# Kernel optimization log

Hardware: AMD Instinct MI355X
Metric: run time of the kernel (lower is better)

## Reference

```python
import jax, jax.numpy as jnp
import numpy as np

N = 102400   # total nodes (256 graphs x 400 nodes)
E = 1600000  # total edges
B = 256      # number of graphs
F_IN = 4
H = 128
GH = 120     # GRU hidden
C_IN = 84
L = 100


def setup_inputs() -> dict:
    key = jax.random.key(0)
    ks = jax.random.split(key, 32)
    rn = lambda k, shape, sc: (jax.random.normal(k, shape, jnp.float32) * sc)
    s = lambda fan: 1.0 / np.sqrt(fan)
    inp = {}
    inp["x"] = rn(ks[0], (N, F_IN), 1.0)
    inp["edge_index"] = jax.random.randint(ks[1], (2, E), 0, N)
    inp["batch"] = jnp.repeat(jnp.arange(B), N // B)  # sorted segment ids, no empty segments
    inp["target01"] = rn(ks[2], (B, C_IN, L), 1.0)
    # GraphConv params: out = segsum(x_j) @ W_rel + b + x @ W_root
    inp["W1_rel"] = rn(ks[3], (F_IN, H), s(F_IN)); inp["W1_root"] = rn(ks[4], (F_IN, H), s(F_IN)); inp["b1"] = jnp.zeros((H,), jnp.float32)
    inp["W2_rel"] = rn(ks[5], (H, H), s(H)); inp["W2_root"] = rn(ks[6], (H, H), s(H)); inp["b2"] = jnp.zeros((H,), jnp.float32)
    inp["W3_rel"] = rn(ks[7], (H, H), s(H)); inp["W3_root"] = rn(ks[8], (H, H), s(H)); inp["b3"] = jnp.zeros((H,), jnp.float32)
    # Conv1d(84 -> 128, k=3)
    inp["Wc"] = rn(ks[9], (H, C_IN, 3), s(C_IN * 3)); inp["bc"] = jnp.zeros((H,), jnp.float32)
    # Bidirectional GRU(128 -> 120)
    inp["Wih_f"] = rn(ks[10], (3 * GH, H), s(H)); inp["Whh_f"] = rn(ks[11], (3 * GH, GH), s(GH))
    inp["bih_f"] = jnp.zeros((3 * GH,), jnp.float32); inp["bhh_f"] = jnp.zeros((3 * GH,), jnp.float32)
    inp["Wih_b"] = rn(ks[12], (3 * GH, H), s(H)); inp["Whh_b"] = rn(ks[13], (3 * GH, GH), s(GH))
    inp["bih_b"] = jnp.zeros((3 * GH,), jnp.float32); inp["bhh_b"] = jnp.zeros((3 * GH,), jnp.float32)
    # Dense head
    inp["Wd1"] = rn(ks[14], (4816, 102), s(4816)); inp["bd1"] = jnp.zeros((102,), jnp.float32)
    inp["Wd3"] = rn(ks[15], (102, 2), s(102)); inp["bd3"] = jnp.zeros((2,), jnp.float32)
    return inp


def _graph_conv(x, src, dst, W_rel, b, W_root, n):
    # PyG GraphConv, aggr='add': lin_rel(sum_j x_j) + lin_root(x)
    agg = jax.ops.segment_sum(x[src], dst, num_segments=n)
    return agg @ W_rel + b + x @ W_root


def _gru_dir(xs, Wih, Whh, bih, bhh, reverse):
    # xs: [T, B, D] -> [T, B, GH]; PyTorch GRU cell equations
    h0 = jnp.zeros((xs.shape[1], Whh.shape[1]), xs.dtype)
    def step(h, xt):
        gi = xt @ Wih.T + bih
        gh = h @ Whh.T + bhh
        ir, iz, i_n = jnp.split(gi, 3, axis=-1)
        hr, hz, h_n = jnp.split(gh, 3, axis=-1)
        r = jax.nn.sigmoid(ir + hr)
        z = jax.nn.sigmoid(iz + hz)
        n = jnp.tanh(i_n + r * h_n)
        h2 = (1.0 - z) * n + z * h
        return h2, h2
    _, ys = jax.lax.scan(step, h0, xs, reverse=reverse)
    return ys


def reference(x, edge_index, batch, target01, W1_rel, W1_root, b1, W2_rel, W2_root, b2,
              W3_rel, W3_root, b3, Wc, bc, Wih_f, Whh_f, bih_f, bhh_f,
              Wih_b, Whh_b, bih_b, bhh_b, Wd1, bd1, Wd3, bd3):
    src, dst = edge_index[0], edge_index[1]
    n = x.shape[0]
    x1 = jax.nn.relu(_graph_conv(x, src, dst, W1_rel, b1, W1_root, n))
    x2 = jax.nn.relu(_graph_conv(x1, src, dst, W2_rel, b2, W2_root, n))
    x3 = jax.nn.relu(_graph_conv(x2, src, dst, W3_rel, b3, W3_root, n)) + x1  # residual
    x4 = jax.nn.relu(_graph_conv(x3, src, dst, W3_rel, b3, W3_root, n))      # conv3 reused
    gmax = jax.ops.segment_max(x4, batch, num_segments=B)
    gsum = jax.ops.segment_sum(x4, batch, num_segments=B)
    cnt = jax.ops.segment_sum(jnp.ones((n, 1), x4.dtype), batch, num_segments=B)
    g = jnp.concatenate([gmax, gsum / cnt], axis=1)  # [B, 256]
    # Conv1d (valid, k=3) + relu
    xl = jax.lax.conv_general_dilated(target01, Wc, (1,), 'VALID',
                                      dimension_numbers=('NCH', 'OIH', 'NCH')) + bc[None, :, None]
    xl = jax.nn.relu(xl)  # [B, 128, 98]
    Lp = (xl.shape[2] // 5) * 5
    xt = xl[:, :, :Lp].reshape(B, H, Lp // 5, 5).mean(-1)  # avg_pool1d k=5 -> [B,128,19]
    xs = jnp.transpose(xt, (2, 0, 1))  # [T, B, 128]
    yf = _gru_dir(xs, Wih_f, Whh_f, bih_f, bhh_f, False)
    yb = _gru_dir(xs, Wih_b, Whh_b, bih_b, bhh_b, True)
    y = jnp.concatenate([yf, yb], axis=-1)            # [T, B, 240]
    y = jnp.transpose(y, (1, 0, 2)).reshape(B, -1)    # [B, 4560]
    xc = jnp.concatenate([g, y], axis=1)              # [B, 4816]
    xc = jax.nn.relu(xc @ Wd1 + bd1)
    return jax.nn.log_softmax(xc @ Wd3 + bd3, axis=-1)
```

## Files before the change

### kernel.cpp

```cpp
#include <hip/hip_runtime.h>
#include <cmath>

constexpr int N_NODES = 102400;
constexpr int N_EDGES = 1600000;
constexpr int BGR     = 256;
constexpr int NPG     = 400;
constexpr int F_IN    = 4;
constexpr int H       = 128;
constexpr int GH      = 120;
constexpr int G3      = 360;
constexpr int C_IN    = 84;
constexpr int LSEQ    = 100;
constexpr int TT      = 19;
constexpr int DHEAD   = 4816;
constexpr int D1O     = 102;
constexpr int KCOMB   = 256;
constexpr int CAP     = 64;
constexpr int NXCD    = 8;
constexpr int NPX     = N_NODES / NXCD;
constexpr int SGRP    = 104;

using short8 = __attribute__((ext_vector_type(8))) short;
using f32x4  = __attribute__((ext_vector_type(4))) float;

__device__ __forceinline__ short f2bf(float f) {
    unsigned u = __float_as_uint(f);
    u += 0x7FFFu + ((u >> 16) & 1u);
    return (short)(u >> 16);
}

__device__ __forceinline__ void tr_seg(const float* __restrict__ in, float* __restrict__ out,
                                       int R, int C, int i) {
    if (i < R * C) {
        int r = i / C, c = i % C;
        out[(long)c * R + r] = in[i];
    }
}
__device__ __forceinline__ void wbt_seg(const float* __restrict__ Wrel, const float* __restrict__ Wroot,
                                        short* __restrict__ WBT, int i) {
    if (i < H * KCOMB) {
        int h = i >> 8, k = i & 255;
        float v = (k < H) ? Wrel[k * H + h] : Wroot[(k - H) * H + h];
        WBT[h * KCOMB + k] = f2bf(v);
    }
}
constexpr int PB0 = 126;
constexpr int PB1 = 180;
constexpr int PB2 = 180;
constexpr int PB3 = 169;
constexpr int PB4 = 169;
constexpr int PB6 = 128;
constexpr int PB7 = 128;
constexpr int PREP_BLOCKS = PB0+PB1+PB2+PB3+PB4+PB6+PB7;

__global__ void prep_fused(const float* Wc, float* WCT,
                           const float* Wihf, float* WIHTF,
                           const float* Wihb, float* WIHTB,
                           const float* Whhf, float* WHHTF,
                           const float* Whhb, float* WHHTB,
                           const float* W2rel, const float* W2root, short* WBT2,
                           const float* W3rel, const float* W3root, short* WBT3) {
    int b = blockIdx.x;
    int t = threadIdx.x;
    if (b < PB0) { tr_seg(Wc,   WCT,   128, 252, b * 256 + t); return; }  b -= PB0;
    if (b < PB1) { tr_seg(Wihf, WIHTF, G3,  H,   b * 256 + t); return; }  b -= PB1;
    if (b < PB2) { tr_seg(Wihb, WIHTB, G3,  H,   b * 256 + t); return; }  b -= PB2;
    if (b < PB3) { tr_seg(Whhf, WHHTF, G3,  GH,  b * 256 + t); return; }  b -= PB3;
    if (b < PB4) { tr_seg(Whhb, WHHTB, G3,  GH,  b * 256 + t); return; }  b -= PB4;
    if (b < PB6) { wbt_seg(W2rel, W2root, WBT2, b * 256 + t); return; }   b -= PB6;
    wbt_seg(W3rel, W3root, WBT3, b * 256 + t);
}

__global__ __launch_bounds__(256) void transpose_tiled(const float* __restrict__ in,
                                                       float* __restrict__ out, int R, int C) {
    __shared__ float tile[32][33];
    const int rb = blockIdx.x * 32, cb = blockIdx.y * 32;
    const int tx = threadIdx.x & 31, ty = threadIdx.x >> 5;
#pragma unroll
    for (int yy = 0; yy < 32; yy += 8) {
        int r = rb + ty + yy, c = cb + tx;
        if (r < R && c < C) tile[ty + yy][tx] = in[(long)r * C + c];
    }
    __syncthreads();
#pragma unroll
    for (int yy = 0; yy < 32; yy += 8) {
        int ro = cb + ty + yy, co = rb + tx;
        if (ro < C && co < R) out[(long)ro * R + co] = tile[tx][ty + yy];
    }
}

__global__ __launch_bounds__(256) void xcd_scatter(const int* __restrict__ src,
                                                   const int* __restrict__ dst,
                                                   int* __restrict__ cnt,
                                                   int* __restrict__ csr, int E) {
    const int g   = blockIdx.x & (NXCD - 1);
    const int grp = blockIdx.x >> 3;
    const int nlo = g * NPX, nhi = nlo + NPX;
    const int stride = SGRP * 256 * 4;
    for (int e = (grp * 256 + threadIdx.x) * 4; e + 3 < E; e += stride) {
        const int4 s = *(const int4*)(src + e);
        const int4 d = *(const int4*)(dst + e);
        if (d.x >= nlo && d.x < nhi) { int p = atomicAdd(&cnt[d.x], 1); csr[((long)d.x << 6) + p] = s.x; }
        if (d.y >= nlo && d.y < nhi) { int p = atomicAdd(&cnt[d.y], 1); csr[((long)d.y << 6) + p] = s.y; }
        if (d.z >= nlo && d.z < nhi) { int p = atomicAdd(&cnt[d.z], 1); csr[((long)d.z << 6) + p] = s.z; }
        if (d.w >= nlo && d.w < nhi) { int p = atomicAdd(&cnt[d.w], 1); csr[((long)d.w << 6) + p] = s.w; }
    }
}

__global__ __launch_bounds__(256) void agg4_csr(const int* __restrict__ cnt,
                                                const int* __restrict__ csr,
                                                const float* __restrict__ x,
                                                float* __restrict__ agg) {
    int i = blockIdx.x * 256 + threadIdx.x;
    int n = i >> 2, c = i & 3;
    const int cn = cnt[n];
    const int* idx = csr + ((long)n << 6);
    float acc = 0.f;
    for (int j = 0; j < cn; ++j) acc += x[(long)idx[j] * 4 + c];
    agg[i] = acc;
}

__global__ void gc1_transform(const float* __restrict__ agg4, const float* __restrict__ x,
                              const float* __restrict__ Wrel, const float* __restrict__ Wroot,
                              const float* __restrict__ bias, float* __restrict__ out) {
    long i = (long)blockIdx.x * 256 + threadIdx.x;
    int h = (int)(i & (H - 1));
    long n = i >> 7;
    const float4 a  = *(const float4*)(agg4 + n * 4);
    const float4 xv = *(const float4*)(x    + n * 4);
    float acc = bias[h]
        + a.x  * Wrel[0 * H + h] + a.y  * Wrel[1 * H + h]
        + a.z  * Wrel[2 * H + h] + a.w  * Wrel[3 * H + h]
        + xv.x * Wroot[0 * H + h] + xv.y * Wroot[1 * H + h]
        + xv.z * Wroot[2 * H + h] + xv.w * Wroot[3 * H + h];
    out[i] = fmaxf(acc, 0.f);
}

__global__ __launch_bounds__(256) void agg128_csr(const int* __restrict__ cnt,
                                                  const int* __restrict__ csr,
                                                  const float* __restrict__ x,
                                                  short* __restrict__ aggb) {
    const int lane = threadIdx.x & 31;
    const int n = blockIdx.x * 8 + (threadIdx.x >> 5);
    const int cn = cnt[n];
    const int* idx = csr + ((long)n << 6);
    float4 acc = make_float4(0.f, 0.f, 0.f, 0.f);
    int j = 0;
    for (; j + 3 < cn; j += 4) {
        const int4 ii = *(const int4*)(idx + j);
        const float4 v0 = *(const float4*)(x + (long)ii.x * H + lane * 4);
        const float4 v1 = *(const float4*)(x + (long)ii.y * H + lane * 4);
        const float4 v2 = *(const float4*)(x + (long)ii.z * H + lane * 4);
        const float4 v3 = *(const float4*)(x + (long)ii.w * H + lane * 4);
        acc.x += (v0.x + v1.x) + (v2.x + v3.x);
        acc.y += (v0.y + v1.y) + (v2.y + v3.y);
        acc.z += (v0.z + v1.z) + (v2.z + v3.z);
        acc.w += (v0.w + v1.w) + (v2.w + v3.w);
    }
    for (; j < cn; ++j) {
        const float4 v0 = *(const float4*)(x + (long)idx[j] * H + lane * 4);
        acc.x += v0.x; acc.y += v0.y; acc.z += v0.z; acc.w += v0.w;
    }
    union { short s[4]; long l; } u;
    u.s[0] = f2bf(acc.x); u.s[1] = f2bf(acc.y);
    u.s[2] = f2bf(acc.z); u.s[3] = f2bf(acc.w);
    *(long*)(aggb + (long)n * H + lane * 4) = u.l;
}

template <int RES>
__global__ __launch_bounds__(256) void gc_mfma(
        const short* __restrict__ aggb, const float* __restrict__ xin,
        const short* __restrict__ WBT, const float* __restrict__ bias,
        const float* __restrict__ res, float* __restrict__ out) {
    const int wid   = threadIdx.x >> 6;
    const int lane  = threadIdx.x & 63;
    const int l15   = lane & 15;
    const int kslot = lane >> 4;
    const long n0   = (long)blockIdx.x * 128 + wid * 32;

    f32x4 acc[2][8];
#pragma unroll
    for (int i = 0; i < 2; ++i)
#pragma unroll
        for (int j = 0; j < 8; ++j) acc[i][j] = (f32x4){0.f, 0.f, 0.f, 0.f};

#pragma unroll
    for (int ks = 0; ks < 8; ++ks) {
        short8 afr[2];
        if (ks < 4) {
            const int koff = ks * 32 + kslot * 8;
#pragma unroll
            for (int rt = 0; rt < 2; ++rt)
                afr[rt] = *(const short8*)(aggb + (n0 + rt * 16 + l15) * H + koff);
        } else {
            const int koff = (ks - 4) * 32 + kslot * 8;
#pragma unroll
            for (int rt = 0; rt < 2; ++rt) {
                const float* p = xin + (n0 + rt * 16 + l15) * H + koff;
                const float4 f0 = *(const float4*)(p);
                const float4 f1 = *(const float4*)(p + 4);
                short8 a;
                a[0] = f2bf(f0.x); a[1] = f2bf(f0.y); a[2] = f2bf(f0.z); a[3] = f2bf(f0.w);
                a[4] = f2bf(f1.x); a[5] = f2bf(f1.y); a[6] = f2bf(f1.z); a[7] = f2bf(f1.w);
                afr[rt] = a;
            }
        }
        const int kb = ks * 32 + kslot * 8;
        short8 bfr[8];
#pragma unroll
        for (int ct = 0; ct < 8; ++ct)
            bfr[ct] = *(const short8*)(WBT + (long)(ct * 16 + l15) * KCOMB + kb);
#pragma unroll
        for (int rt = 0; rt < 2; ++rt)
#pragma unroll
            for (int ct = 0; ct < 8; ++ct)
                acc[rt][ct] = __builtin_amdgcn_mfma_f32_16x16x32_bf16(
                    afr[rt], bfr[ct], acc[rt][ct], 0, 0, 0);
    }

#pragma unroll
    for (int rt = 0; rt < 2; ++rt) {
        const long rbase = n0 + rt * 16 + kslot * 4;
#pragma unroll
        for (int ct = 0; ct < 8; ++ct) {
            const int h = ct * 16 + l15;
            const float bv = bias[h];
#pragma unroll
            for (int r = 0; r < 4; ++r) {
                const long rowi = rbase + r;
                float v = fmaxf(acc[rt][ct][r] + bv, 0.f);
                if (RES) v += res[rowi * H + h];
                out[rowi * H + h] = v;
            }
        }
    }
}

__global__ __launch_bounds__(512) void pool_kernel(const float* __restrict__ x4, float* __restrict__ xc) {
    int g = blockIdx.x;
    int h = threadIdx.x & 127;
    int part = threadIdx.x >> 7;
    const float* base = x4 + ((long)g * NPG + part * 100) * H + h;
    float mx = -INFINITY, sm = 0.f;
#pragma unroll 4
    for (int i = 0; i < 100; ++i) {
        float v = base[(long)i * H];
        mx = fmaxf(mx, v);
        sm += v;
    }
    __shared__ float smx[4][128], ssm[4][128];
    smx[part][h] = mx; ssm[part][h] = sm;
    __syncthreads();
    if (part == 0) {
        float m = fmaxf(fmaxf(smx[0][h], smx[1][h]), fmaxf(smx[2][h], smx[3][h]));
        float s = ssm[0][h] + ssm[1][h] + ssm[2][h] + ssm[3][h];
        xc[(long)g * DHEAD + h] = m;
        xc[(long)g * DHEAD + H + h] = s * (1.f / NPG);
    }
}

__global__ __launch_bounds__(128) void conv1d_pool(const float* __restrict__ in,
                                                   const float* __restrict__ WcT,
                                                   const float* __restrict__ bc,
                                                   float* __restrict__ xs) {
    int p = blockIdx.x;
    int b = blockIdx.y;
    int o = threadIdx.x;
    __shared__ float sIn[C_IN][8];
    const float* ib = in + (long)b * C_IN * LSEQ;
    for (int idx = threadIdx.x; idx < C_IN * 7; idx += 128) {
        int c = idx / 7, j = idx % 7;
        sIn[c][j] = ib[c * LSEQ + 5 * p + j];
    }
    __syncthreads();
    float a0 = 0, a1 = 0, a2 = 0, a3 = 0, a4 = 0;
    for (int c = 0; c < C_IN; ++c) {
        float i0 = sIn[c][0], i1 = sIn[c][1], i2 = sIn[c][2], i3 = sIn[c][3];
        float i4 = sIn[c][4], i5 = sIn[c][5], i6 = sIn[c][6];
        float w0 = WcT[(c * 3 + 0) * H + o];
        float w1 = WcT[(c * 3 + 1) * H + o];
        float w2 = WcT[(c * 3 + 2) * H + o];
        a0 += w0 * i0 + w1 * i1 + w2 * i2;
        a1 += w0 * i1 + w1 * i2 + w2 * i3;
        a2 += w0 * i2 + w1 * i3 + w2 * i4;
        a3 += w0 * i3 + w1 * i4 + w2 * i5;
        a4 += w0 * i4 + w1 * i5 + w2 * i6;
    }
    float bcv = bc[o];
    float r = fmaxf(a0 + bcv, 0.f) + fmaxf(a1 + bcv, 0.f) + fmaxf(a2 + bcv, 0.f)
            + fmaxf(a3 + bcv, 0.f) + fmaxf(a4 + bcv, 0.f);
    xs[((long)p * BGR + b) * H + o] = r * 0.2f;
}

__global__ __launch_bounds__(384) void gi_gemm(const float* __restrict__ xs,
                                               const float* __restrict__ WihT,
                                               const float* __restrict__ bih,
                                               float* __restrict__ gi) {
    const long r0 = (long)blockIdx.x * 16;
    const int g = threadIdx.x;
    __shared__ __align__(16) float sX[16][H];
    for (int idx = threadIdx.x; idx < 16 * H; idx += 384)
        sX[idx >> 7][idx & (H - 1)] = xs[r0 * H + idx];
    __syncthreads();
    if (g >= G3) return;
    const float bv = bih[g];
    float acc[16];
#pragma unroll
    for (int r = 0; r < 16; ++r) acc[r] = bv;
    for (int k = 0; k < H; k += 4) {
        float w0 = WihT[(k + 0) * G3 + g], w1 = WihT[(k + 1) * G3 + g];
        float w2 = WihT[(k + 2) * G3 + g], w3 = WihT[(k + 3) * G3 + g];
#pragma unroll
        for (int r = 0; r < 16; ++r) {
            float4 xv = *(const float4*)&sX[r][k];
            acc[r] += xv.x * w0 + xv.y * w1 + xv.z * w2 + xv.w * w3;
        }
    }
#pragma unroll
    for (int r = 0; r < 16; ++r)
        gi[(r0 + r) * G3 + g] = acc[r];
}

__device__ __forceinline__ float sigmoidf_(float x) { return 1.f / (1.f + expf(-x)); }

__global__ __launch_bounds__(384) void gru_kernel(
        const float* __restrict__ giF, const float* __restrict__ giB,
        const float* __restrict__ WhhTF, const float* __restrict__ WhhTB,
        const float* __restrict__ bhhF, const float* __restrict__ bhhB,
        float* __restrict__ xc) {
    const int b = blockIdx.x & (BGR - 1);
    const int dir = blockIdx.x >> 8;
    const float* gi   = dir ? giB : giF;
    const float* WhhT = dir ? WhhTB : WhhTF;
    const float* bhh  = dir ? bhhB : bhhF;
    const int g = threadIdx.x;
    const int gc = g < G3 ? g : (G3 - 1);

    float w[GH];
#pragma unroll
    for (int k = 0; k < GH; ++k) w[k] = WhhT[(long)k * G3 + gc];
    const float bh = bhh[gc];

    __shared__ __align__(16) float sh[GH];
    __shared__ float sgh[G3];
    if (g < GH) sh[g] = 0.f;
    __syncthreads();

    for (int tt = 0; tt < TT; ++tt) {
        const int t = dir ? (TT - 1 - tt) : tt;
        float acc = bh;
#pragma unroll
        for (int k4 = 0; k4 < GH / 4; ++k4) {
            float4 hv = *(const float4*)&sh[k4 * 4];
            acc += hv.x * w[k4 * 4] + hv.y * w[k4 * 4 + 1]
                 + hv.z * w[k4 * 4 + 2] + hv.w * w[k4 * 4 + 3];
        }
        if (g < G3) sgh[g] = acc;
        __syncthreads();
        if (g < GH) {
            const float* gib = gi + ((long)t * BGR + b) * G3;
            float r = sigmoidf_(gib[g] + sgh[g]);
            float z = sigmoidf_(gib[GH + g] + sgh[GH + g]);
            float n = tanhf(gib[2 * GH + g] + r * sgh[2 * GH + g]);
            float h2 = (1.f - z) * n + z * sh[g];
            sh[g] = h2;
            xc[(long)b * DHEAD + 256 + t * 240 + dir * GH + g] = h2;
        }
        __syncthreads();
    }
}

__global__ __launch_bounds__(256) void dense1(const float* __restrict__ xc,
                                              const float* __restrict__ Wd1T,
                                              const float* __restrict__ bd1,
                                              float* __restrict__ d1) {
    const int wid  = blockIdx.x * 4 + (threadIdx.x >> 6);
    const int lane = threadIdx.x & 63;
    const int jg = wid % 26;
    const int bg = wid / 26;
    const int j0 = jg * 4, b0 = bg * 8;

    float acc[4][8];
#pragma unroll
    for (int jj = 0; jj < 4; ++jj)
#pragma unroll
        for (int bb = 0; bb < 8; ++bb) acc[jj][bb] = 0.f;

    for (int i = lane; i < DHEAD / 4; i += 64) {
        float4 wv[4], xv[8];
#pragma unroll
        for (int jj = 0; jj < 4; ++jj) {
            int j = j0 + jj; if (j > D1O - 1) j = D1O - 1;
            wv[jj] = *(const float4*)(Wd1T + (long)j * DHEAD + i * 4);
        }
#pragma unroll
        for (int bb = 0; bb < 8; ++bb)
            xv[bb] = *(const float4*)(xc + (long)(b0 + bb) * DHEAD + i * 4);
#pragma unroll
        for (int jj = 0; jj < 4; ++jj)
#pragma unroll
            for (int bb = 0; bb < 8; ++bb)
                acc[jj][bb] += wv[jj].x * xv[bb].x + wv[jj].y * xv[bb].y
                             + wv[jj].z * xv[bb].z + wv[jj].w * xv[bb].w;
    }
#pragma unroll
    for (int m = 32; m >= 1; m >>= 1)
#pragma unroll
        for (int jj = 0; jj < 4; ++jj)
#pragma unroll
            for (int bb = 0; bb < 8; ++bb)
                acc[jj][bb] += __shfl_xor(acc[jj][bb], m, 64);
    if (lane < 32) {
        const int jj = lane >> 3, bb = lane & 7;
        const int j = j0 + jj;
        if (j < D1O)
            d1[(long)(b0 + bb) * D1O + j] = fmaxf(acc[jj][bb] + bd1[j], 0.f);
    }
}

__global__ void final_head(const float* __restrict__ d1, const float* __restrict__ Wd3,
                           const float* __restrict__ bd3, float* __restrict__ out) {
    int b = threadIdx.x;
    if (b >= BGR) return;
    float v0 = bd3[0], v1 = bd3[1];
    for (int k = 0; k < D1O; ++k) {
        float xv = d1[(long)b * D1O + k];
        v0 += xv * Wd3[k * 2 + 0];
        v1 += xv * Wd3[k * 2 + 1];
    }
    float m = fmaxf(v0, v1);
    float lse = m + logf(expf(v0 - m) + expf(v1 - m));
    out[b * 2 + 0] = v0 - lse;
    out[b * 2 + 1] = v1 - lse;
}

extern "C" void kernel_launch(void* const* d_in, const int* in_sizes, int n_in,
                              void* d_out, int out_size, void* d_ws, size_t ws_size,
                              hipStream_t stream) {
    const float* x      = (const float*)d_in[0];
    const int*   ei     = (const int*)d_in[1];
    const float* tgt    = (const float*)d_in[3];
    const float* W1rel  = (const float*)d_in[4];
    const float* W1root = (const float*)d_in[5];
    const float* b1     = (const float*)d_in[6];
    const float* W2rel  = (const float*)d_in[7];
    const float* W2root = (const float*)d_in[8];
    const float* b2     = (const float*)d_in[9];
    const float* W3rel  = (const float*)d_in[10];
    const float* W3root = (const float*)d_in[11];
    const float* b3     = (const float*)d_in[12];
    const float* Wc     = (const float*)d_in[13];
    const float* bc     = (const float*)d_in[14];
    const float* Wih_f  = (const float*)d_in[15];
    const float* Whh_f  = (const float*)d_in[16];
    const float* bih_f  = (const float*)d_in[17];
    const float* bhh_f  = (const float*)d_in[18];
    const float* Wih_b  = (const float*)d_in[19];
    const float* Whh_b  = (const float*)d_in[20];
    const float* bih_b  = (const float*)d_in[21];
    const float* bhh_b  = (const float*)d_in[22];
    const float* Wd1    = (const float*)d_in[23];
    const float* bd1    = (const float*)d_in[24];
    const float* Wd3    = (const float*)d_in[25];
    const float* bd3    = (const float*)d_in[26];

    const int* srcI = ei;
    const int* dstI = ei + N_EDGES;

    float* ws = (float*)d_ws;
    size_t off = 0;
    float* AGG4  = ws + off; off += (size_t)N_NODES * 4;
    float* X1    = ws + off; off += (size_t)N_NODES * H;
    float* BUFA  = ws + off; off += (size_t)N_NODES * H;
    float* BUFB  = ws + off; off += (size_t)N_NODES * H;
    float* XS    = ws + off; off += (size_t)TT * BGR * H;
    float* GIF   = ws + off; off += (size_t)TT * BGR * G3;
    float* GIB   = ws + off; off += (size_t)TT * BGR * G3;
    float* XC    = ws + off; off += (size_t)BGR * DHEAD;
    float* D1    = ws + off; off += (size_t)BGR * D1O + 2;
    float* WCT   = ws + off; off += (size_t)C_IN * 3 * H;
    float* WIHTF = ws + off; off += (size_t)H * G3;
    float* WIHTB = ws + off; off += (size_t)H * G3;
    float* WHHTF = ws + off; off += (size_t)GH * G3;
    float* WHHTB = ws + off; off += (size_t)GH * G3;
    float* WD1T  = ws + off; off += (size_t)DHEAD * D1O;
    off = (off + 3) & ~(size_t)3;
    short* WBT2  = (short*)(ws + off); off += (size_t)H * KCOMB / 2;
    short* WBT3  = (short*)(ws + off); off += (size_t)H * KCOMB / 2;
    short* AGGB  = (short*)(ws + off); off += (size_t)N_NODES * H / 2;
    int* ibase   = (int*)(ws + off);
    int* CNT     = ibase;
    int* CSR     = ibase + N_NODES;

    prep_fused<<<PREP_BLOCKS, 256, 0, stream>>>(Wc, WCT, Wih_f, WIHTF, Wih_b, WIHTB,
                                                Whh_f, WHHTF, Whh_b, WHHTB,
                                                W2rel, W2root, WBT2, W3rel, W3root, WBT3);
    transpose_tiled<<<dim3((DHEAD + 31) / 32, (D1O + 31) / 32), 256, 0, stream>>>(Wd1, WD1T, DHEAD, D1O);

    hipMemsetAsync(CNT, 0, (size_t)N_NODES * sizeof(int), stream);
    xcd_scatter<<<NXCD * SGRP, 256, 0, stream>>>(srcI, dstI, CNT, CSR, N_EDGES);

    agg4_csr<<<(N_NODES * 4) / 256, 256, 0, stream>>>(CNT, CSR, x, AGG4);
    gc1_transform<<<(N_NODES * H) / 256, 256, 0, stream>>>(AGG4, x, W1rel, W1root, b1, X1);

    agg128_csr<<<N_NODES / 8, 256, 0, stream>>>(CNT, CSR, X1, AGGB);
    gc_mfma<0><<<N_NODES / 128, 256, 0, stream>>>(AGGB, X1, WBT2, b2, nullptr, BUFA);

    agg128_csr<<<N_NODES / 8, 256, 0, stream>>>(CNT, CSR, BUFA, AGGB);
    gc_mfma<1><<<N_NODES / 128, 256, 0, stream>>>(AGGB, BUFA, WBT3, b3, X1, BUFB);

    agg128_csr<<<N_NODES / 8, 256, 0, stream>>>(CNT, CSR, BUFB, AGGB);
    gc_mfma<0><<<N_NODES / 128, 256, 0, stream>>>(AGGB, BUFB, WBT3, b3, nullptr, X1);

    pool_kernel<<<BGR, 512, 0, stream>>>(X1, XC);

    conv1d_pool<<<dim3(TT, BGR), 128, 0, stream>>>(tgt, WCT, bc, XS);

    gi_gemm<<<(TT * BGR) / 16, 384, 0, stream>>>(XS, WIHTF, bih_f, GIF);
    gi_gemm<<<(TT * BGR) / 16, 384, 0, stream>>>(XS, WIHTB, bih_b, GIB);

    gru_kernel<<<2 * BGR, 384, 0, stream>>>(GIF, GIB, WHHTF, WHHTB, bhh_f, bhh_b, XC);

    dense1<<<(26 * 32) / 4, 256, 0, stream>>>(XC, WD1T, bd1, D1);
    final_head<<<1, 256, 0, stream>>>(D1, Wd3, bd3, (float*)d_out);
}
```

Before: 818.2 us.

## Store intermediate node features in bf16 for gather and MFMA inputs

The GraphConv layers now write bf16 copies of their activations, and the neighbor aggregation gathers bf16 rows (16 lanes × 8 elements) instead of fp32 rows. This halves the bytes moved by the random-access gather, which dominates the graph layers. The MFMA kernel now reads the bf16 root-input directly, with no per-element conversion, and writes only the outputs needed downstream. In exchange, the neighbor sums are built from bf16-rounded values, which adds rounding error, and an extra bf16 store is added in gc1.

```diff
diff --git a/kernel.cpp b/kernel.cpp
--- a/kernel.cpp
+++ b/kernel.cpp
@@ -28,6 +28,9 @@
     u += 0x7FFFu + ((u >> 16) & 1u);
     return (short)(u >> 16);
 }
+__device__ __forceinline__ float bf2f(short s) {
+    return __uint_as_float(((unsigned)(unsigned short)s) << 16);
+}
 
 __device__ __forceinline__ void tr_seg(const float* __restrict__ in, float* __restrict__ out,
                                        int R, int C, int i) {
@@ -122,7 +125,8 @@
 
 __global__ void gc1_transform(const float* __restrict__ agg4, const float* __restrict__ x,
                               const float* __restrict__ Wrel, const float* __restrict__ Wroot,
-                              const float* __restrict__ bias, float* __restrict__ out) {
+                              const float* __restrict__ bias, float* __restrict__ out,
+                              short* __restrict__ outb) {
     long i = (long)blockIdx.x * 256 + threadIdx.x;
     int h = (int)(i & (H - 1));
     long n = i >> 7;
@@ -133,45 +137,50 @@
         + a.z  * Wrel[2 * H + h] + a.w  * Wrel[3 * H + h]
         + xv.x * Wroot[0 * H + h] + xv.y * Wroot[1 * H + h]
         + xv.z * Wroot[2 * H + h] + xv.w * Wroot[3 * H + h];
-    out[i] = fmaxf(acc, 0.f);
-}
-
-__global__ __launch_bounds__(256) void agg128_csr(const int* __restrict__ cnt,
-                                                  const int* __restrict__ csr,
-                                                  const float* __restrict__ x,
-                                                  short* __restrict__ aggb) {
-    const int lane = threadIdx.x & 31;
-    const int n = blockIdx.x * 8 + (threadIdx.x >> 5);
+    float v = fmaxf(acc, 0.f);
+    out[i] = v;
+    outb[i] = f2bf(v);
+}
+
+__global__ __launch_bounds__(256) void agg128_bf(const int* __restrict__ cnt,
+                                                 const int* __restrict__ csr,
+                                                 const short* __restrict__ xb,
+                                                 short* __restrict__ aggb) {
+    const int lane = threadIdx.x & 15;
+    const int n = blockIdx.x * 16 + (threadIdx.x >> 4);
     const int cn = cnt[n];
     const int* idx = csr + ((long)n << 6);
-    float4 acc = make_float4(0.f, 0.f, 0.f, 0.f);
+    float acc[8];
+#pragma unroll
+    for (int q = 0; q < 8; ++q) acc[q] = 0.f;
     int j = 0;
     for (; j + 3 < cn; j += 4) {
         const int4 ii = *(const int4*)(idx + j);
-        const float4 v0 = *(const float4*)(x + (long)ii.x * H + lane * 4);
-        const float4 v1 = *(const float4*)(x + (long)ii.y * H + lane * 4);
-        const float4 v2 = *(const float4*)(x + (long)ii.z * H + lane * 4);
-        const float4 v3 = *(const float4*)(x + (long)ii.w * H + lane * 4);
-        acc.x += (v0.x + v1.x) + (v2.x + v3.x);
-        acc.y += (v0.y + v1.y) + (v2.y + v3.y);
-        acc.z += (v0.z + v1.z) + (v2.z + v3.z);
-        acc.w += (v0.w + v1.w) + (v2.w + v3.w);
+        const short8 r0 = *(const short8*)(xb + (long)ii.x * H + lane * 8);
+        const short8 r1 = *(const short8*)(xb + (long)ii.y * H + lane * 8);
+        const short8 r2 = *(const short8*)(xb + (long)ii.z * H + lane * 8);
+        const short8 r3 = *(const short8*)(xb + (long)ii.w * H + lane * 8);
+#pragma unroll
+        for (int q = 0; q < 8; ++q)
+            acc[q] += (bf2f(r0[q]) + bf2f(r1[q])) + (bf2f(r2[q]) + bf2f(r3[q]));
     }
     for (; j < cn; ++j) {
-        const float4 v0 = *(const float4*)(x + (long)idx[j] * H + lane * 4);
-        acc.x += v0.x; acc.y += v0.y; acc.z += v0.z; acc.w += v0.w;
-    }
-    union { short s[4]; long l; } u;
-    u.s[0] = f2bf(acc.x); u.s[1] = f2bf(acc.y);
-    u.s[2] = f2bf(acc.z); u.s[3] = f2bf(acc.w);
-    *(long*)(aggb + (long)n * H + lane * 4) = u.l;
-}
-
-template <int RES>
+        const short8 r0 = *(const short8*)(xb + (long)idx[j] * H + lane * 8);
+#pragma unroll
+        for (int q = 0; q < 8; ++q) acc[q] += bf2f(r0[q]);
+    }
+    short8 o;
+#pragma unroll
+    for (int q = 0; q < 8; ++q) o[q] = f2bf(acc[q]);
+    *(short8*)(aggb + (long)n * H + lane * 8) = o;
+}
+
+template <int RES, int OUTF, int OUTB>
 __global__ __launch_bounds__(256) void gc_mfma(
-        const short* __restrict__ aggb, const float* __restrict__ xin,
+        const short* __restrict__ aggb, const short* __restrict__ xinb,
         const short* __restrict__ WBT, const float* __restrict__ bias,
-        const float* __restrict__ res, float* __restrict__ out) {
+        const float* __restrict__ res, float* __restrict__ outf,
+        short* __restrict__ outb) {
     const int wid   = threadIdx.x >> 6;
     const int lane  = threadIdx.x & 63;
     const int l15   = lane & 15;
@@ -186,25 +195,12 @@
 
 #pragma unroll
     for (int ks = 0; ks < 8; ++ks) {
+        const short* srcb = (ks < 4) ? aggb : xinb;
+        const int koff = (ks < 4 ? ks * 32 : (ks - 4) * 32) + kslot * 8;
         short8 afr[2];
-        if (ks < 4) {
-            const int koff = ks * 32 + kslot * 8;
-#pragma unroll
-            for (int rt = 0; rt < 2; ++rt)
-                afr[rt] = *(const short8*)(aggb + (n0 + rt * 16 + l15) * H + koff);
-        } else {
-            const int koff = (ks - 4) * 32 + kslot * 8;
-#pragma unroll
-            for (int rt = 0; rt < 2; ++rt) {
-                const float* p = xin + (n0 + rt * 16 + l15) * H + koff;
-                const float4 f0 = *(const float4*)(p);
-                const float4 f1 = *(const float4*)(p + 4);
-                short8 a;
-                a[0] = f2bf(f0.x); a[1] = f2bf(f0.y); a[2] = f2bf(f0.z); a[3] = f2bf(f0.w);
-                a[4] = f2bf(f1.x); a[5] = f2bf(f1.y); a[6] = f2bf(f1.z); a[7] = f2bf(f1.w);
-                afr[rt] = a;
-            }
-        }
+#pragma unroll
+        for (int rt = 0; rt < 2; ++rt)
+            afr[rt] = *(const short8*)(srcb + (n0 + rt * 16 + l15) * H + koff);
         const int kb = ks * 32 + kslot * 8;
         short8 bfr[8];
 #pragma unroll
@@ -230,7 +226,8 @@
                 const long rowi = rbase + r;
                 float v = fmaxf(acc[rt][ct][r] + bv, 0.f);
                 if (RES) v += res[rowi * H + h];
-                out[rowi * H + h] = v;
+                if (OUTF) outf[rowi * H + h] = v;
+                if (OUTB) outb[rowi * H + h] = f2bf(v);
             }
         }
     }
@@ -471,8 +468,6 @@
     size_t off = 0;
     float* AGG4  = ws + off; off += (size_t)N_NODES * 4;
     float* X1    = ws + off; off += (size_t)N_NODES * H;
-    float* BUFA  = ws + off; off += (size_t)N_NODES * H;
-    float* BUFB  = ws + off; off += (size_t)N_NODES * H;
     float* XS    = ws + off; off += (size_t)TT * BGR * H;
     float* GIF   = ws + off; off += (size_t)TT * BGR * G3;
     float* GIB   = ws + off; off += (size_t)TT * BGR * G3;
@@ -488,6 +483,9 @@
     short* WBT2  = (short*)(ws + off); off += (size_t)H * KCOMB / 2;
     short* WBT3  = (short*)(ws + off); off += (size_t)H * KCOMB / 2;
     short* AGGB  = (short*)(ws + off); off += (size_t)N_NODES * H / 2;
+    short* X1B   = (short*)(ws + off); off += (size_t)N_NODES * H / 2;
+    short* X2B   = (short*)(ws + off); off += (size_t)N_NODES * H / 2;
+    short* X3B   = (short*)(ws + off); off += (size_t)N_NODES * H / 2;
     int* ibase   = (int*)(ws + off);
     int* CNT     = ibase;
     int* CSR     = ibase + N_NODES;
@@ -501,16 +499,16 @@
     xcd_scatter<<<NXCD * SGRP, 256, 0, stream>>>(srcI, dstI, CNT, CSR, N_EDGES);
 
     agg4_csr<<<(N_NODES * 4) / 256, 256, 0, stream>>>(CNT, CSR, x, AGG4);
-    gc1_transform<<<(N_NODES * H) / 256, 256, 0, stream>>>(AGG4, x, W1rel, W1root, b1, X1);
-
-    agg128_csr<<<N_NODES / 8, 256, 0, stream>>>(CNT, CSR, X1, AGGB);
-    gc_mfma<0><<<N_NODES / 128, 256, 0, stream>>>(AGGB, X1, WBT2, b2, nullptr, BUFA);
-
-    agg128_csr<<<N_NODES / 8, 256, 0, stream>>>(CNT, CSR, BUFA, AGGB);
-    gc_mfma<1><<<N_NODES / 128, 256, 0, stream>>>(AGGB, BUFA, WBT3, b3, X1, BUFB);
-
-    agg128_csr<<<N_NODES / 8, 256, 0, stream>>>(CNT, CSR, BUFB, AGGB);
-    gc_mfma<0><<<N_NODES / 128, 256, 0, stream>>>(AGGB, BUFB, WBT3, b3, nullptr, X1);
+    gc1_transform<<<(N_NODES * H) / 256, 256, 0, stream>>>(AGG4, x, W1rel, W1root, b1, X1, X1B);
+
+    agg128_bf<<<N_NODES / 16, 256, 0, stream>>>(CNT, CSR, X1B, AGGB);
+    gc_mfma<0, 0, 1><<<N_NODES / 128, 256, 0, stream>>>(AGGB, X1B, WBT2, b2, nullptr, nullptr, X2B);
+
+    agg128_bf<<<N_NODES / 16, 256, 0, stream>>>(CNT, CSR, X2B, AGGB);
+    gc_mfma<1, 0, 1><<<N_NODES / 128, 256, 0, stream>>>(AGGB, X2B, WBT3, b3, X1, nullptr, X3B);
+
+    agg128_bf<<<N_NODES / 16, 256, 0, stream>>>(CNT, CSR, X3B, AGGB);
+    gc_mfma<0, 1, 0><<<N_NODES / 128, 256, 0, stream>>>(AGGB, X3B, WBT3, b3, nullptr, X1, nullptr);
 
     pool_kernel<<<BGR, 512, 0, stream>>>(X1, XC);
 
```

After: 714.3 us. -12.7%, faster.
